# Kernel optimization log

Measured on AMD Instinct MI355X. Metric: run time of the kernel, lower is better.

Reference implementation:

```python
import jax, jax.numpy as jnp
import numpy as np

B, S, HID = 2, 2048, 2048
H, HD, RD, LD = 16, 128, 64, 512
AD = HD + RD  # attn_dim = 192
SCALE = 1.0 / np.sqrt(AD)


def apply_rope(x):
    """x: [B, H, S, RD] -> RoPE-rotated, matching the torch RotaryEmbedding."""
    s = x.shape[2]
    inv_freq = 1.0 / (10000.0 ** (jnp.arange(0, RD, 2, dtype=jnp.float32) / RD))
    t = jnp.arange(s, dtype=x.dtype)
    freqs = t[:, None] * inv_freq[None, :]          # [S, RD//2]
    cos, sin = jnp.cos(freqs), jnp.sin(freqs)       # broadcast over B, H
    x1, x2 = x[..., : RD // 2], x[..., RD // 2 :]
    return jnp.concatenate([x1 * cos - x2 * sin, x2 * cos + x1 * sin], axis=-1)


def setup_inputs() -> dict:
    key = jax.random.key(0)
    ks = jax.random.split(key, 7)
    std = 0.02
    return {
        "x": jax.random.normal(ks[0], (B, S, HID), jnp.float32),
        # weights stored as [in, out] (transpose of torch Linear.weight)
        "wq": jax.random.normal(ks[1], (HID, H * HD), jnp.float32) * std,
        "wq_rope": jax.random.normal(ks[2], (HID, H * RD), jnp.float32) * std,
        "wkv_down": jax.random.normal(ks[3], (HID, LD), jnp.float32) * std,
        "wkv_up": jax.random.normal(ks[4], (LD, H * 2 * HD), jnp.float32) * std,
        "wk_rope": jax.random.normal(ks[5], (HID, RD), jnp.float32) * std,
        "wo": jax.random.normal(ks[6], (H * AD, HID), jnp.float32) * std,
    }


def reference(x, wq, wq_rope, wkv_down, wkv_up, wk_rope, wo):
    b, s, _ = x.shape
    # query paths
    q_nope = (x @ wq).reshape(b, s, H, HD).transpose(0, 2, 1, 3)        # [B,H,S,HD]
    q_rope = (x @ wq_rope).reshape(b, s, H, RD).transpose(0, 2, 1, 3)   # [B,H,S,RD]
    q_rope = apply_rope(q_rope)
    q = jnp.concatenate([q_nope, q_rope], axis=-1)                      # [B,H,S,AD]
    # low-rank KV latent upcast
    kv_latent = x @ wkv_down                                            # [B,S,LD]
    kv = (kv_latent @ wkv_up).reshape(b, s, H, 2 * HD).transpose(0, 2, 1, 3)
    k_nope, v = kv[..., :HD], kv[..., HD:]                              # [B,H,S,HD]
    # shared rope key, broadcast over heads
    k_rope = jnp.broadcast_to((x @ wk_rope)[:, None], (b, H, s, RD))
    k_rope = apply_rope(k_rope)
    k = jnp.concatenate([k_nope, k_rope], axis=-1)                      # [B,H,S,AD]
    # zero-pad V to attn_dim
    v_pad = jnp.pad(v, ((0, 0), (0, 0), (0, 0), (0, RD)))
    # attention (causal)
    scores = jnp.einsum("bhqd,bhkd->bhqk", q, k) * SCALE
    causal = jnp.tril(jnp.ones((s, s), bool))
    scores = jnp.where(causal, scores, jnp.finfo(scores.dtype).min)
    probs = jax.nn.softmax(scores, axis=-1)
    attn = jnp.einsum("bhqk,bhkd->bhqd", probs, v_pad)                  # [B,H,S,AD]
    attn = attn.transpose(0, 2, 1, 3).reshape(b, s, H * AD)
    return attn @ wo
```

## Files before the change

### kernel.cpp

```cpp
#include <hip/hip_runtime.h>
#include <math.h>

#define HB 2
#define HS 2048
#define HHID 2048
#define HH 16
#define HHD 128
#define HRD 64
#define HLD 512
#define HAD 192
#define HM (HB*HS)

static __device__ __constant__ float C1_SCALE_LOG2E = 0.1041175465f;

typedef unsigned short US;
typedef __attribute__((ext_vector_type(8))) short s8v;
typedef __attribute__((ext_vector_type(4))) float f4v;
typedef __attribute__((ext_vector_type(16))) float f16v;

#if __has_builtin(__builtin_amdgcn_exp2f)
#define EXP2F __builtin_amdgcn_exp2f
#else
#define EXP2F exp2f
#endif

__device__ __forceinline__ US f2b(float f){
  union { float f; unsigned u; } v; v.f = f;
  unsigned r = v.u + 0x7fffu + ((v.u >> 16) & 1u);
  return (US)(r >> 16);
}
__device__ __forceinline__ float b2f(US u){
  union { unsigned u; float f; } v; v.u = ((unsigned)u) << 16; return v.f;
}
__device__ __forceinline__ f4v mfma16(s8v a, s8v b, f4v c){
  return __builtin_amdgcn_mfma_f32_16x16x32_bf16(a, b, c, 0, 0, 0);
}
__device__ __forceinline__ f16v mfma32(s8v a, s8v b, f16v c){
  return __builtin_amdgcn_mfma_f32_32x32x16_bf16(a, b, c, 0, 0, 0);
}
__device__ __forceinline__ void gload_lds16(const void* g, void* l){
  __builtin_amdgcn_global_load_lds((const __attribute__((address_space(1))) void*)g,
                                   (__attribute__((address_space(3))) void*)l, 16, 0, 0);
}

__global__ __launch_bounds__(256) void k_cast(const float* __restrict__ in, US* __restrict__ out, int n){
  int i = (blockIdx.x * 256 + threadIdx.x) * 4;
  if (i >= n) return;
  float4 v = *(const float4*)(in + i);
  union { US q[4]; unsigned u[2]; } p;
  p.q[0] = f2b(v.x); p.q[1] = f2b(v.y); p.q[2] = f2b(v.z); p.q[3] = f2b(v.w);
  *(uint2*)(out + i) = make_uint2(p.u[0], p.u[1]);
}

__global__ __launch_bounds__(256) void k_rope_tab(float2* __restrict__ tab){
  int idx = blockIdx.x * 256 + threadIdx.x;
  int s = idx >> 5, i = idx & 31;
  float invf = expf(-9.210340371976184f * (float)i / 32.f);
  float fr = (float)s * invf;
  tab[idx] = make_float2(cosf(fr), sinf(fr));
}

template<int WOMAP>
__global__ __launch_bounds__(256) void k_transpose_cast(const float* __restrict__ W, US* __restrict__ Wt, int K, int N){
  __shared__ float t[32][33];
  int n0 = blockIdx.x * 32, k0 = blockIdx.y * 32;
  int tx = threadIdx.x, ty = threadIdx.y;
  #pragma unroll
  for (int r = 0; r < 32; r += 8){
    int k = k0 + ty + r;
    int sk = WOMAP ? ((k >> 7) * 192 + (k & 127)) : k;
    t[ty + r][tx] = W[(size_t)sk * N + n0 + tx];
  }
  __syncthreads();
  #pragma unroll
  for (int r = 0; r < 32; r += 8){
    Wt[(size_t)(n0 + ty + r) * K + k0 + tx] = f2b(t[tx][ty + r]);
  }
}

__global__ __launch_bounds__(256) void k_transpose_v(const US* __restrict__ v, US* __restrict__ vT){
  __shared__ US t[32][33];
  int bh = blockIdx.z;
  int s0 = blockIdx.x * 32, d0 = blockIdx.y * 32;
  const US* src = v + (size_t)bh * HS * HHD;
  US* dst = vT + (size_t)bh * HHD * HS;
  int tx = threadIdx.x, ty = threadIdx.y;
  #pragma unroll
  for (int r = 0; r < 32; r += 8)
    t[ty + r][tx] = src[(size_t)(s0 + ty + r) * HHD + d0 + tx];
  __syncthreads();
  #pragma unroll
  for (int r = 0; r < 32; r += 8)
    dst[(size_t)(d0 + ty + r) * HS + s0 + tx] = t[tx][ty + r];
}

template<int EPI>
__global__ __launch_bounds__(256, 2) void k_gemm2(
    const US* __restrict__ A, const US* __restrict__ Bt,
    void* __restrict__ out0, void* __restrict__ out1,
    void* __restrict__ out2, void* __restrict__ out3,
    int Kdim, int Ndim)
{
  __shared__ US As[2][128 * 64];
  __shared__ US Bs[2][128 * 64];
  const int tid = threadIdx.x;
  const int lane = tid & 63, w = tid >> 6;
  const int r15 = lane & 15, kh = lane >> 4;
  const int gx = gridDim.x;
  const int flat = blockIdx.y * gx + blockIdx.x;
  const int cpx = (gx * gridDim.y) >> 3;
  const int swz = (flat & 7) * cpx + (flat >> 3);
  const int m0 = (swz / gx) * 128, n0 = (swz % gx) * 128;
  const int wm = (w >> 1) * 64, wn = (w & 1) * 64;
  const int rsw = (r15 & 7) << 4;
  f4v acc[4][4] = {};

  auto STAGE = [&](int k0, int bb){
    #pragma unroll
    for (int j = 0; j < 4; ++j){
      int c = j * 256 + tid;
      int row = c >> 3, colD = (c & 7) * 16;
      gload_lds16((const char*)A + ((size_t)(m0 + row) * Kdim + k0) * 2 + (colD ^ ((row & 7) << 4)),
                  (char*)As[bb] + c * 16);
    }
    #pragma unroll
    for (int j = 0; j < 4; ++j){
      int c = j * 256 + tid;
      int row = c >> 3, colD = (c & 7) * 16;
      gload_lds16((const char*)Bt + ((size_t)(n0 + row) * Kdim + k0) * 2 + (colD ^ ((row & 7) << 4)),
                  (char*)Bs[bb] + c * 16);
    }
  };

  const int nk = Kdim >> 6;
  STAGE(0, 0);
  for (int t = 0; t < nk; ++t){
    if (t + 1 < nk){
      STAGE((t + 1) * 64, (t + 1) & 1);
      asm volatile("s_waitcnt vmcnt(8)" ::: "memory");
    } else {
      asm volatile("s_waitcnt vmcnt(0)" ::: "memory");
    }
    __builtin_amdgcn_s_barrier();
    __builtin_amdgcn_sched_barrier(0);
    const char* AB = (const char*)As[t & 1];
    const char* BB = (const char*)Bs[t & 1];
    #pragma unroll
    for (int ks = 0; ks < 2; ++ks){
      s8v af[4];
      #pragma unroll
      for (int mi = 0; mi < 4; ++mi)
        af[mi] = *(const s8v*)(AB + (wm + mi * 16 + r15) * 128 + ((ks * 64 + kh * 16) ^ rsw));
      #pragma unroll
      for (int ni = 0; ni < 4; ++ni){
        s8v bf = *(const s8v*)(BB + (wn + ni * 16 + r15) * 128 + ((ks * 64 + kh * 16) ^ rsw));
        #pragma unroll
        for (int mi = 0; mi < 4; ++mi)
          acc[mi][ni] = mfma16(af[mi], bf, acc[mi][ni]);
      }
    }
    __builtin_amdgcn_s_barrier();
  }

  #pragma unroll
  for (int mi = 0; mi < 4; ++mi){
    #pragma unroll
    for (int ni = 0; ni < 4; ++ni){
      #pragma unroll
      for (int j = 0; j < 4; ++j){
        float v = acc[mi][ni][j];
        int m = m0 + wm + mi * 16 + kh * 4 + j;
        int n = n0 + wn + ni * 16 + r15;
        if (EPI == 3){
          int b = m >> 11, s = m & 2047;
          int h = n >> 8, r = n & 255;
          if (r < 128)
            ((US*)out0)[((size_t)(b * HH + h) * HS + s) * HHD + r] = f2b(v);
          else
            ((US*)out1)[((size_t)(b * HH + h) * HS + s) * HHD + (r - 128)] = f2b(v);
        } else if (EPI == 4){
          ((float*)out0)[(size_t)m * HHID + n] = v;
        } else {
          int b = m >> 11, s = m & 2047;
          if (n < 2048){
            int h = n >> 7, d = n & 127;
            ((US*)out0)[((size_t)(b * HH + h) * HS + s) * HAD + d] = f2b(v);
          } else if (n < 3072){
            int dd2 = n - 2048;
            int h = dd2 >> 6, dd = dd2 & 63;
            float partner = acc[mi][ni ^ 2][j];
            float2 cs = ((const float2*)out1)[s * 32 + (dd & 31)];
            float o = (dd < 32) ? (v * cs.x - partner * cs.y) : (v * cs.x + partner * cs.y);
            ((US*)out0)[((size_t)(b * HH + h) * HS + s) * HAD + HHD + dd] = f2b(o);
          } else if (n < 3584){
            ((US*)out2)[(size_t)m * HLD + (n - 3072)] = f2b(v);
          } else if (n < 3648){
            int dd = n - 3584;
            float partner = acc[mi][ni ^ 2][j];
            float2 cs = ((const float2*)out1)[s * 32 + (dd & 31)];
            float o = (dd < 32) ? (v * cs.x - partner * cs.y) : (v * cs.x + partner * cs.y);
            ((US*)out3)[(size_t)m * HRD + dd] = f2b(o);
          }
        }
      }
    }
  }
}

__global__ __launch_bounds__(256, 2) void k_attn(
    const US* __restrict__ qbuf, const US* __restrict__ knbuf,
    const US* __restrict__ krbuf, const US* __restrict__ vT,
    US* __restrict__ attnb)
{
  __shared__ US Ks[2][64 * 192];
  __shared__ US Vs[2][128 * 64];

  const int tid = threadIdx.x, lane = tid & 63, w = tid >> 6;
  const int l31 = lane & 31, hi = lane >> 5;
  const int bid = blockIdx.x;
  const int bh = bid & 31, b = bh >> 4, head = bh & 15;
  const int u = (bid < 256) ? (15 - (bid >> 5)) : ((bid - 256) >> 5);
  const int q0 = u * 128;
  const int qw0 = q0 + w * 32;
  const int qrow = qw0 + l31;
  const int sw = (l31 & 7) << 4;

  const char* qb = (const char*)(qbuf + (size_t)bh * HS * HAD);
  const char* kn = (const char*)(knbuf + (size_t)bh * HS * HHD);
  const char* kr = (const char*)(krbuf + (size_t)b * HS * HRD);
  const char* vb = (const char*)(vT   + (size_t)bh * HHD * HS);

  s8v qf[12];
  {
    const char* qr = qb + (size_t)qrow * 384;
    #pragma unroll
    for (int ks = 0; ks < 12; ++ks)
      qf[ks] = *(const s8v*)(qr + ks * 32 + hi * 16);
  }

  auto STAGE = [&](int tt, int bb){
    const int k0s = tt * 64;
    #pragma unroll
    for (int j = 0; j < 6; ++j){
      int c = j * 256 + tid;
      int row = c / 24, cc = c - row * 24;
      int xsw = (row & 7) << 4;
      const char* src = (cc < 16)
          ? kn + (size_t)(k0s + row) * 256 + ((cc * 16) ^ xsw)
          : kr + (size_t)(k0s + row) * 128 + (((cc - 16) * 16) ^ xsw);
      gload_lds16(src, (char*)Ks[bb] + (j * 4 + w) * 1024);
    }
    #pragma unroll
    for (int j = 0; j < 4; ++j){
      int c = j * 256 + tid;
      int d = c >> 3, colD = (c & 7) * 16;
      gload_lds16(vb + (size_t)d * (HS * 2) + (size_t)k0s * 2 + (colD ^ ((d & 7) << 4)),
                  (char*)Vs[bb] + (j * 4 + w) * 1024);
    }
  };

  f16v acc_o[4] = {};
  float mraw = -3e38f, lsum = 0.f;

  const int nt = (q0 + 128) >> 6;
  STAGE(0, 0);
  for (int t = 0; t < nt; ++t){
    if (t + 1 < nt){
      STAGE(t + 1, (t + 1) & 1);
      asm volatile("s_waitcnt vmcnt(10)" ::: "memory");
    } else {
      asm volatile("s_waitcnt vmcnt(0)" ::: "memory");
    }
    __builtin_amdgcn_s_barrier();
    __builtin_amdgcn_sched_barrier(0);

    const int k0 = t * 64;
    if (k0 <= qw0 + 31){
      const char* KB = (const char*)Ks[t & 1];
      const char* VB = (const char*)Vs[t & 1];
      f16v sacc[2] = {};
      #pragma unroll
      for (int ks = 0; ks < 12; ++ks){
        #pragma unroll
        for (int ni = 0; ni < 2; ++ni){
          s8v kf = *(const s8v*)(KB + (ni * 32 + l31) * 384 + ((ks * 32 + hi * 16) ^ sw));
          sacc[ni] = mfma32(kf, qf[ks], sacc[ni]);
        }
      }

      const bool need_mask = (k0 + 63 > qrow);
      float mx = -3e38f;
      #pragma unroll
      for (int ni = 0; ni < 2; ++ni){
        #pragma unroll
        for (int r = 0; r < 16; ++r){
          float s = sacc[ni][r];
          if (need_mask){
            int kv = k0 + ni * 32 + (r & 3) + 8 * (r >> 2) + 4 * hi;
            if (kv > qrow) s = -3e38f;
            sacc[ni][r] = s;
          }
          mx = fmaxf(mx, s);
        }
      }
      mx = fmaxf(mx, __shfl_xor(mx, 32));

      float scl = 1.0f;
      if (__any(mx > mraw + 76.8f)){
        float mnew = fmaxf(mraw, mx);
        scl = EXP2F((mraw - mnew) * C1_SCALE_LOG2E);
        mraw = mnew;
        #pragma unroll
        for (int r = 0; r < 16; ++r){
          float sb = __shfl(scl, (r & 3) + 8 * (r >> 2) + 4 * hi);
          #pragma unroll
          for (int db = 0; db < 4; ++db)
            acc_o[db][r] *= sb;
        }
      }

      float m2 = mraw * C1_SCALE_LOG2E;
      float rs = 0.f;
      #pragma unroll
      for (int ni = 0; ni < 2; ++ni){
        #pragma unroll
        for (int r = 0; r < 16; ++r){
          float p = EXP2F(fmaf(sacc[ni][r], C1_SCALE_LOG2E, -m2));
          sacc[ni][r] = p;
          rs += p;
        }
      }
      rs += __shfl_xor(rs, 32);
      lsum = lsum * scl + rs;

      union PU { s8v v; unsigned u[4]; } pa[4];
      #pragma unroll
      for (int ni = 0; ni < 2; ++ni){
        #pragma unroll
        for (int g = 0; g < 2; ++g){
          unsigned a0, a1, b0, b1;
          const int rb = g * 8;
          asm("v_cvt_pk_bf16_f32 %0, %1, %2" : "=v"(a0) : "v"(sacc[ni][rb + 0]), "v"(sacc[ni][rb + 1]));
          asm("v_cvt_pk_bf16_f32 %0, %1, %2" : "=v"(a1) : "v"(sacc[ni][rb + 2]), "v"(sacc[ni][rb + 3]));
          asm("v_cvt_pk_bf16_f32 %0, %1, %2" : "=v"(b0) : "v"(sacc[ni][rb + 4]), "v"(sacc[ni][rb + 5]));
          asm("v_cvt_pk_bf16_f32 %0, %1, %2" : "=v"(b1) : "v"(sacc[ni][rb + 6]), "v"(sacc[ni][rb + 7]));
          asm("v_permlane32_swap_b32 %0, %1" : "+v"(a0), "+v"(b0));
          asm("v_permlane32_swap_b32 %0, %1" : "+v"(a1), "+v"(b1));
          pa[ni * 2 + g].u[0] = a0; pa[ni * 2 + g].u[1] = a1;
          pa[ni * 2 + g].u[2] = b0; pa[ni * 2 + g].u[3] = b1;
        }
      }

      #pragma unroll
      for (int ks2 = 0; ks2 < 4; ++ks2){
        #pragma unroll
        for (int db = 0; db < 4; ++db){
          s8v vf = *(const s8v*)(VB + (db * 32 + l31) * 128 + ((ks2 * 32 + hi * 16) ^ sw));
          acc_o[db] = mfma32(pa[ks2].v, vf, acc_o[db]);
        }
      }
    }
    __builtin_amdgcn_s_barrier();
  }

  float linv = 1.0f / lsum;
  #pragma unroll
  for (int r = 0; r < 16; ++r){
    int crow = (r & 3) + 8 * (r >> 2) + 4 * hi;
    float lb = __shfl(linv, crow);
    int qq = qw0 + crow;
    US* dst = attnb + (size_t)(b * HS + qq) * (HH * HHD) + head * HHD;
    #pragma unroll
    for (int db = 0; db < 4; ++db)
      dst[db * 32 + l31] = f2b(acc_o[db][r] * lb);
  }
}

extern "C" void kernel_launch(void* const* d_in, const int* in_sizes, int n_in,
                              void* d_out, int out_size, void* d_ws, size_t ws_size,
                              hipStream_t stream)
{
  (void)in_sizes; (void)n_in; (void)out_size; (void)ws_size;
  const float* x        = (const float*)d_in[0];
  const float* wq       = (const float*)d_in[1];
  const float* wq_rope  = (const float*)d_in[2];
  const float* wkv_down = (const float*)d_in[3];
  const float* wkv_up   = (const float*)d_in[4];
  const float* wk_rope  = (const float*)d_in[5];
  const float* wo       = (const float*)d_in[6];

  char* ws = (char*)d_ws;
  size_t off = 0;
  auto alloc = [&](size_t bytes)->void*{ void* p = ws + off; off += (bytes + 255) & ~(size_t)255; return p; };

  US* xb     = (US*)alloc((size_t)HM * HHID * 2);
  US* wqT    = (US*)alloc((size_t)2048 * 2048 * 2);
  US* wqrT   = (US*)alloc((size_t)1024 * 2048 * 2);
  US* wkvdT  = (US*)alloc((size_t)512 * 2048 * 2);
  US* wkrT   = (US*)alloc((size_t)64 * 2048 * 2);
  US* wkrPad = (US*)alloc((size_t)64 * 2048 * 2);
  US* wkvuT  = (US*)alloc((size_t)4096 * 512 * 2);
  US* woT    = (US*)alloc((size_t)2048 * 2048 * 2);
  US* qbuf   = (US*)alloc((size_t)32 * HS * HAD * 2);
  US* knbuf  = (US*)alloc((size_t)32 * HS * HHD * 2);
  US* krbuf  = (US*)alloc((size_t)HB * HS * HRD * 2);
  US* vbuf   = (US*)alloc((size_t)32 * HS * HHD * 2);
  US* vTb    = (US*)alloc((size_t)32 * HS * HHD * 2);
  US* latent = (US*)alloc((size_t)HM * HLD * 2);
  float2* tab = (float2*)alloc((size_t)HS * 32 * 8);
  US* attnb = xb;

  dim3 tb(256);
  dim3 t328(32, 8);

  hipMemsetAsync(wkrPad, 0, (size_t)64 * 2048 * 2, stream);
  k_cast<<<dim3(8192), tb, 0, stream>>>(x, xb, HM * HHID);
  k_rope_tab<<<dim3(256), tb, 0, stream>>>(tab);
  k_transpose_cast<0><<<dim3(64, 64),  t328, 0, stream>>>(wq,       wqT,   2048, 2048);
  k_transpose_cast<0><<<dim3(32, 64),  t328, 0, stream>>>(wq_rope,  wqrT,  2048, 1024);
  k_transpose_cast<0><<<dim3(16, 64),  t328, 0, stream>>>(wkv_down, wkvdT, 2048, 512);
  k_transpose_cast<0><<<dim3(128, 16), t328, 0, stream>>>(wkv_up,   wkvuT, 512,  4096);
  k_transpose_cast<0><<<dim3(2, 64),   t328, 0, stream>>>(wk_rope,  wkrT,  2048, 64);
  k_transpose_cast<1><<<dim3(64, 64),  t328, 0, stream>>>(wo,       woT,   2048, 2048);

  k_gemm2<5><<<dim3(29, 32), tb, 0, stream>>>(xb, wqT, (void*)qbuf, (void*)tab, (void*)latent, (void*)krbuf, 2048, 3712);
  k_gemm2<3><<<dim3(32, 32), tb, 0, stream>>>(latent, wkvuT, (void*)knbuf, (void*)vbuf, (void*)nullptr, (void*)nullptr, 512, 4096);
  k_transpose_v<<<dim3(64, 4, 32), t328, 0, stream>>>(vbuf, vTb);
  k_attn<<<dim3(512), tb, 0, stream>>>(qbuf, knbuf, krbuf, vTb, attnb);
  k_gemm2<4><<<dim3(16, 32), tb, 0, stream>>>(attnb, woT, d_out, (void*)nullptr, (void*)nullptr, (void*)nullptr, 2048, 2048);
}
```

Before: 292.4 us.

## Add 256x256 eight-wave pipelined GEMM for projection and KV-up GEMMs

Adds a new GEMM kernel with 512 threads and 256x256 output tiles, double-buffered LDS staged by direct global-to-LDS loads. Loads are interleaved across four MFMA phases using barriers, setprio and explicit vmcnt waits. The fused Q/latent/k_rope projection and the KV up-projection now use this kernel, with N padded to 3840 and the zero-pad weight buffer grown to match. Larger tiles increase reuse per load but cut the grid to 240 or 256 blocks, which may leave CUs underused and adds padding work.

```diff
diff --git a/kernel.cpp b/kernel.cpp
--- a/kernel.cpp
+++ b/kernel.cpp
@@ -171,6 +171,143 @@
         float v = acc[mi][ni][j];
         int m = m0 + wm + mi * 16 + kh * 4 + j;
         int n = n0 + wn + ni * 16 + r15;
+        if (EPI == 4){
+          ((float*)out0)[(size_t)m * HHID + n] = v;
+        }
+      }
+    }
+  }
+}
+
+template<int EPI>
+__global__ __launch_bounds__(512, 1) void k_gemm8(
+    const US* __restrict__ A, const US* __restrict__ Bt,
+    void* __restrict__ out0, void* __restrict__ out1,
+    void* __restrict__ out2, void* __restrict__ out3,
+    int Kdim, int Ndim)
+{
+  __shared__ US As[2][256 * 64];
+  __shared__ US Bs[2][256 * 64];
+  const int tid = threadIdx.x, lane = tid & 63, w = tid >> 6;
+  const int r15 = lane & 15, kh = lane >> 4;
+  const int gx = gridDim.x;
+  const int flat = blockIdx.y * gx + blockIdx.x;
+  const int cpx = (gx * gridDim.y) >> 3;
+  const int swz = (flat & 7) * cpx + (flat >> 3);
+  const int m0 = (swz / gx) * 256, n0 = (swz % gx) * 256;
+  const int wmL = (w >> 2) * 128, wnL = (w & 3) * 64;
+  const int rsw = (r15 & 7) << 4;
+  const int nt = Kdim >> 6;
+
+  f4v acc[8][4] = {};
+  s8v bf[4][2];
+
+  auto STAGE_A = [&](int t, int par, int half){
+    int tt = (t < nt) ? t : (nt - 1);
+    #pragma unroll
+    for (int j = 0; j < 2; ++j){
+      int c = j * 512 + tid;
+      int row = c >> 3, ch = c & 7;
+      gload_lds16((const char*)A + ((size_t)(m0 + half * 128 + row) * Kdim + tt * 64) * 2 + ((ch * 16) ^ ((row & 7) << 4)),
+                  (char*)As[par] + half * 16384 + c * 16);
+    }
+  };
+  auto STAGE_B = [&](int t, int par, int half){
+    int tt = (t < nt) ? t : (nt - 1);
+    #pragma unroll
+    for (int j = 0; j < 2; ++j){
+      int c = j * 512 + tid;
+      int row = c >> 3, ch = c & 7;
+      gload_lds16((const char*)Bt + ((size_t)(n0 + half * 128 + row) * Kdim + tt * 64) * 2 + ((ch * 16) ^ ((row & 7) << 4)),
+                  (char*)Bs[par] + half * 16384 + c * 16);
+    }
+  };
+
+  STAGE_B(0, 0, 0); STAGE_B(0, 0, 1);
+  STAGE_A(0, 0, 0); STAGE_A(0, 0, 1);
+  STAGE_B(1, 1, 0); STAGE_B(1, 1, 1);
+  asm volatile("s_waitcnt vmcnt(4)" ::: "memory");
+  __builtin_amdgcn_s_barrier();
+
+  const int nk2 = nt >> 1;
+  for (int i = 0; i < nk2; ++i){
+    const int t0 = 2 * i, t1 = 2 * i + 1;
+    #pragma unroll
+    for (int p = 0; p < 4; ++p){
+      if (p == 0){
+        #pragma unroll
+        for (int ni = 0; ni < 4; ++ni)
+          #pragma unroll
+          for (int kk = 0; kk < 2; ++kk)
+            bf[ni][kk] = *(const s8v*)((const char*)Bs[0] + (wnL + ni * 16 + r15) * 128 + ((kk * 64 + kh * 16) ^ rsw));
+      }
+      s8v af[2][2];
+      #pragma unroll
+      for (int m2 = 0; m2 < 2; ++m2)
+        #pragma unroll
+        for (int kk = 0; kk < 2; ++kk)
+          af[m2][kk] = *(const s8v*)((const char*)As[0] + (wmL + (p * 2 + m2) * 16 + r15) * 128 + ((kk * 64 + kh * 16) ^ rsw));
+      if (p == 0){ STAGE_A(t1, 1, 0); }
+      else if (p == 1){ STAGE_A(t1, 1, 1); STAGE_B(t0 + 2, 0, 0); }
+      else if (p == 2){ STAGE_B(t0 + 2, 0, 1); }
+      __builtin_amdgcn_s_barrier();
+      __builtin_amdgcn_sched_barrier(0);
+      __builtin_amdgcn_s_setprio(1);
+      #pragma unroll
+      for (int m2 = 0; m2 < 2; ++m2)
+        #pragma unroll
+        for (int ni = 0; ni < 4; ++ni)
+          #pragma unroll
+          for (int kk = 0; kk < 2; ++kk)
+            acc[p * 2 + m2][ni] = mfma16(af[m2][kk], bf[ni][kk], acc[p * 2 + m2][ni]);
+      __builtin_amdgcn_s_setprio(0);
+      if (p == 3){ asm volatile("s_waitcnt vmcnt(4)" ::: "memory"); }
+      __builtin_amdgcn_s_barrier();
+    }
+    #pragma unroll
+    for (int p = 0; p < 4; ++p){
+      if (p == 0){
+        #pragma unroll
+        for (int ni = 0; ni < 4; ++ni)
+          #pragma unroll
+          for (int kk = 0; kk < 2; ++kk)
+            bf[ni][kk] = *(const s8v*)((const char*)Bs[1] + (wnL + ni * 16 + r15) * 128 + ((kk * 64 + kh * 16) ^ rsw));
+      }
+      s8v af[2][2];
+      #pragma unroll
+      for (int m2 = 0; m2 < 2; ++m2)
+        #pragma unroll
+        for (int kk = 0; kk < 2; ++kk)
+          af[m2][kk] = *(const s8v*)((const char*)As[1] + (wmL + (p * 2 + m2) * 16 + r15) * 128 + ((kk * 64 + kh * 16) ^ rsw));
+      if (p == 0){ STAGE_A(t0 + 2, 0, 0); }
+      else if (p == 1){ STAGE_A(t0 + 2, 0, 1); }
+      else if (p == 2){ STAGE_B(t1 + 2, 1, 0); }
+      else if (p == 3){ STAGE_B(t1 + 2, 1, 1); }
+      __builtin_amdgcn_s_barrier();
+      __builtin_amdgcn_sched_barrier(0);
+      __builtin_amdgcn_s_setprio(1);
+      #pragma unroll
+      for (int m2 = 0; m2 < 2; ++m2)
+        #pragma unroll
+        for (int ni = 0; ni < 4; ++ni)
+          #pragma unroll
+          for (int kk = 0; kk < 2; ++kk)
+            acc[p * 2 + m2][ni] = mfma16(af[m2][kk], bf[ni][kk], acc[p * 2 + m2][ni]);
+      __builtin_amdgcn_s_setprio(0);
+      if (p == 3){ asm volatile("s_waitcnt vmcnt(4)" ::: "memory"); }
+      __builtin_amdgcn_s_barrier();
+    }
+  }
+
+  #pragma unroll
+  for (int mi = 0; mi < 8; ++mi){
+    #pragma unroll
+    for (int ni = 0; ni < 4; ++ni){
+      #pragma unroll
+      for (int j = 0; j < 4; ++j){
+        float v = acc[mi][ni][j];
+        int m = m0 + wmL + mi * 16 + kh * 4 + j;
+        int n = n0 + wnL + ni * 16 + r15;
         if (EPI == 3){
           int b = m >> 11, s = m & 2047;
           int h = n >> 8, r = n & 255;
@@ -178,8 +315,6 @@
             ((US*)out0)[((size_t)(b * HH + h) * HS + s) * HHD + r] = f2b(v);
           else
             ((US*)out1)[((size_t)(b * HH + h) * HS + s) * HHD + (r - 128)] = f2b(v);
-        } else if (EPI == 4){
-          ((float*)out0)[(size_t)m * HHID + n] = v;
         } else {
           int b = m >> 11, s = m & 2047;
           if (n < 2048){
@@ -398,7 +533,7 @@
   US* wqrT   = (US*)alloc((size_t)1024 * 2048 * 2);
   US* wkvdT  = (US*)alloc((size_t)512 * 2048 * 2);
   US* wkrT   = (US*)alloc((size_t)64 * 2048 * 2);
-  US* wkrPad = (US*)alloc((size_t)64 * 2048 * 2);
+  US* wkrPad = (US*)alloc((size_t)192 * 2048 * 2);
   US* wkvuT  = (US*)alloc((size_t)4096 * 512 * 2);
   US* woT    = (US*)alloc((size_t)2048 * 2048 * 2);
   US* qbuf   = (US*)alloc((size_t)32 * HS * HAD * 2);
@@ -413,7 +548,7 @@
   dim3 tb(256);
   dim3 t328(32, 8);
 
-  hipMemsetAsync(wkrPad, 0, (size_t)64 * 2048 * 2, stream);
+  hipMemsetAsync(wkrPad, 0, (size_t)192 * 2048 * 2, stream);
   k_cast<<<dim3(8192), tb, 0, stream>>>(x, xb, HM * HHID);
   k_rope_tab<<<dim3(256), tb, 0, stream>>>(tab);
   k_transpose_cast<0><<<dim3(64, 64),  t328, 0, stream>>>(wq,       wqT,   2048, 2048);
@@ -423,8 +558,8 @@
   k_transpose_cast<0><<<dim3(2, 64),   t328, 0, stream>>>(wk_rope,  wkrT,  2048, 64);
   k_transpose_cast<1><<<dim3(64, 64),  t328, 0, stream>>>(wo,       woT,   2048, 2048);
 
-  k_gemm2<5><<<dim3(29, 32), tb, 0, stream>>>(xb, wqT, (void*)qbuf, (void*)tab, (void*)latent, (void*)krbuf, 2048, 3712);
-  k_gemm2<3><<<dim3(32, 32), tb, 0, stream>>>(latent, wkvuT, (void*)knbuf, (void*)vbuf, (void*)nullptr, (void*)nullptr, 512, 4096);
+  k_gemm8<5><<<dim3(15, 16), dim3(512), 0, stream>>>(xb, wqT, (void*)qbuf, (void*)tab, (void*)latent, (void*)krbuf, 2048, 3840);
+  k_gemm8<3><<<dim3(16, 16), dim3(512), 0, stream>>>(latent, wkvuT, (void*)knbuf, (void*)vbuf, (void*)nullptr, (void*)nullptr, 512, 4096);
   k_transpose_v<<<dim3(64, 4, 32), t328, 0, stream>>>(vbuf, vTb);
   k_attn<<<dim3(512), tb, 0, stream>>>(qbuf, knbuf, krbuf, vTb, attnb);
   k_gemm2<4><<<dim3(16, 32), tb, 0, stream>>>(attnb, woT, d_out, (void*)nullptr, (void*)nullptr, (void*)nullptr, 2048, 2048);
```

Measured after the change: 277.8 us. 5.0% less time.
